# Performance work log

Hardware: AMD Instinct MI355X
Metric: run time of the kernel (lower is better)

Reference implementation:

```python
import jax, jax.numpy as jnp
import numpy as np

B, L, D = 2, 1024, 2048
E, K = 8, 2
H, HS = 1408, 2816


def setup_inputs() -> dict:
    key = jax.random.key(0)
    ks = jax.random.split(key, 9)
    s = 0.02  # param init scale
    return {
        "x": jax.random.normal(ks[0], (B, L, D), dtype=jnp.float32),
        "gate_w": jax.random.normal(ks[1], (E, D), dtype=jnp.float32) * s,
        "w_gate": jax.random.normal(ks[2], (E, D, H), dtype=jnp.float32) * s,
        "w_up": jax.random.normal(ks[3], (E, D, H), dtype=jnp.float32) * s,
        "w_down": jax.random.normal(ks[4], (E, H, D), dtype=jnp.float32) * s,
        "shgate_w": jax.random.normal(ks[5], (D,), dtype=jnp.float32) * s,
        "shw_gate": jax.random.normal(ks[6], (D, HS), dtype=jnp.float32) * s,
        "shw_up": jax.random.normal(ks[7], (D, HS), dtype=jnp.float32) * s,
        "shw_down": jax.random.normal(ks[8], (HS, D), dtype=jnp.float32) * s,
    }


def reference(x, gate_w, w_gate, w_up, w_down, shgate_w, shw_gate, shw_up, shw_down):
    b, l, d = x.shape
    xf = x.reshape(-1, d)  # [T, D]

    # --- router: softmax over expert logits, top-k, renormalize ---
    logits = jnp.einsum("td,ed->te", xf.astype(jnp.float32), gate_w)
    probs = jax.nn.softmax(logits.astype(jnp.float32), axis=-1)  # [T, E]
    weights, indices = jax.lax.top_k(probs, K)                   # [T, K]
    weights = (weights / weights.sum(-1, keepdims=True)).astype(x.dtype)

    # per-token combine weight for each expert: sum of top-k weights routed to e
    onehot = jax.nn.one_hot(indices, E, dtype=x.dtype)           # [T, K, E]
    combine = jnp.einsum("tk,tke->te", weights, onehot)          # [T, E]

    # --- experts (dense vectorized equivalent of masked gather/scatter loop) ---
    g = jnp.einsum("td,edh->teh", xf, w_gate)
    u = jnp.einsum("td,edh->teh", xf, w_up)
    h = jax.nn.silu(g) * u                                       # [T, E, H]
    # fused down-proj + weighted combine; accumulate in fp32 like the original
    out = jnp.einsum("teh,ehd,te->td", h.astype(jnp.float32),
                     w_down.astype(jnp.float32), combine.astype(jnp.float32))

    # --- shared expert with sigmoid gate ---
    sgate = jax.nn.sigmoid(xf @ shgate_w)[:, None]               # [T, 1]
    sh = (jax.nn.silu(xf @ shw_gate) * (xf @ shw_up)) @ shw_down  # [T, D]
    out = out + (sgate * sh).astype(jnp.float32)

    return out.astype(x.dtype).reshape(b, l, d)
```

## Files before the change

kernel.cpp:

```cpp
#include <hip/hip_runtime.h>
#include <hip/hip_bf16.h>
#include <math.h>

#define T_TOK 2048
#define Dd    2048
#define Ee    8
#define Hh    1408
#define HSs   2816
#define CAP   1024

typedef __attribute__((ext_vector_type(8))) __bf16 bf16x8;
typedef __attribute__((ext_vector_type(4))) __bf16 bf16x4;
typedef __attribute__((ext_vector_type(2))) __bf16 bf16x2;
typedef __attribute__((ext_vector_type(4))) float  f32x4;

#define MFMA(a, b, c) __builtin_amdgcn_mfma_f32_16x16x32_bf16(a, b, c, 0, 0, 0)

__device__ __forceinline__ void async_copy16(const __bf16* g, __bf16* l) {
    __builtin_amdgcn_global_load_lds(
        (const __attribute__((address_space(1))) unsigned int*)g,
        (__attribute__((address_space(3))) unsigned int*)l, 16, 0, 0);
}

__global__ void init_cnt(int* __restrict__ cnt) {
    if (threadIdx.x < Ee) cnt[threadIdx.x] = 0;
}

__global__ __launch_bounds__(256) void router_kernel(
    const float* __restrict__ x, const float* __restrict__ gate_w,
    const float* __restrict__ shgate_w,
    int* __restrict__ cnt, int* __restrict__ ptok, int* __restrict__ pslot,
    float* __restrict__ pw, float* __restrict__ sgate)
{
    const int t = blockIdx.x;
    const int tid = threadIdx.x;
    const float* xt = x + (size_t)t * Dd;

    float acc[Ee];
#pragma unroll
    for (int e = 0; e < Ee; e++) acc[e] = 0.f;
    float accs = 0.f;

    for (int d = tid; d < Dd; d += 256) {
        float xv = xt[d];
#pragma unroll
        for (int e = 0; e < Ee; e++) acc[e] += xv * gate_w[e * Dd + d];
        accs += xv * shgate_w[d];
    }

    __shared__ float red[Ee + 1][256];
#pragma unroll
    for (int e = 0; e < Ee; e++) red[e][tid] = acc[e];
    red[Ee][tid] = accs;
    __syncthreads();

    for (int s = 128; s > 0; s >>= 1) {
        if (tid < s) {
#pragma unroll
            for (int e = 0; e <= Ee; e++) red[e][tid] += red[e][tid + s];
        }
        __syncthreads();
    }

    if (tid == 0) {
        float l0 = -1e30f, l1 = -1e30f;
        int i0 = 0, i1 = 0;
#pragma unroll
        for (int e = 0; e < Ee; e++) {
            float v = red[e][0];
            if (v > l0) { l1 = l0; i1 = i0; l0 = v; i0 = e; }
            else if (v > l1) { l1 = v; i1 = e; }
        }
        float w0 = 1.f / (1.f + expf(l1 - l0));
        float w1 = 1.f - w0;

        int p0 = atomicAdd(&cnt[i0], 1);
        if (p0 < CAP) {
            ptok[i0 * CAP + p0] = t; pslot[i0 * CAP + p0] = 2 * t;
            pw[i0 * CAP + p0] = w0;
        }
        int p1 = atomicAdd(&cnt[i1], 1);
        if (p1 < CAP) {
            ptok[i1 * CAP + p1] = t; pslot[i1 * CAP + p1] = 2 * t + 1;
            pw[i1 * CAP + p1] = w1;
        }
        sgate[t] = 1.f / (1.f + expf(-red[Ee][0]));
    }
}

__global__ __launch_bounds__(256) void cvt_x(const float* __restrict__ src,
                                             __bf16* __restrict__ dst)
{
    int i = blockIdx.x * 256 + threadIdx.x;
    float4 v = ((const float4*)src)[i];
    bf16x4 o = { (__bf16)v.x, (__bf16)v.y, (__bf16)v.z, (__bf16)v.w };
    ((bf16x4*)dst)[i] = o;
}

__global__ __launch_bounds__(256) void transpose_cvt(
    const float* __restrict__ src, __bf16* __restrict__ dst, int R, int C)
{
    src += (size_t)blockIdx.z * R * C;
    dst += (size_t)blockIdx.z * R * C;
    __shared__ float tile[64][65];
    const int tid = threadIdx.x, tx = tid & 63, ty = tid >> 6;
    const int c0 = blockIdx.x * 64, r0 = blockIdx.y * 64;
#pragma unroll
    for (int j = 0; j < 16; j++) {
        int r = j * 4 + ty;
        tile[r][tx] = src[(size_t)(r0 + r) * C + c0 + tx];
    }
    __syncthreads();
    const int rp = (tid & 31) * 2;
    const int cg = tid >> 5;
#pragma unroll
    for (int j = 0; j < 8; j++) {
        int c = j * 8 + cg;
        bf16x2 v = { (__bf16)tile[rp][c], (__bf16)tile[rp + 1][c] };
        *(bf16x2*)&dst[(size_t)(c0 + c) * R + r0 + rp] = v;
    }
}

__global__ __launch_bounds__(256, 3) void gateup_all(
    const __bf16* __restrict__ xb,
    const __bf16* __restrict__ wgT, const __bf16* __restrict__ wuT,
    const __bf16* __restrict__ shwgT, const __bf16* __restrict__ shwuT,
    const int* __restrict__ cnt, const int* __restrict__ ptok,
    __bf16* __restrict__ hq, __bf16* __restrict__ shh)
{
    const int bx = blockIdx.x;
    const int tid = threadIdx.x, lane = tid & 63, wave = tid >> 6;
    const int wr = wave >> 1, wc = wave & 1;
    const int lm = lane & 15, lq = lane >> 4;

    bool sh;
    int m0, h0, n, e = 0;
    const __bf16 *bg_mat, *bu_mat;
    if (bx < 1408) {
        sh = false;
        int mtg = bx / 22, ht = bx - mtg * 22;
        e = mtg >> 3; m0 = (mtg & 7) * 128; h0 = ht * 64;
        n = cnt[e]; if (n > CAP) n = CAP;
        if (m0 >= n) return;
        bg_mat = wgT + (size_t)e * Hh * Dd;
        bu_mat = wuT + (size_t)e * Hh * Dd;
    } else {
        sh = true;
        int s = bx - 1408;
        int mt = s / 44, ht = s - mt * 44;
        m0 = mt * 128; h0 = ht * 64; n = T_TOK;
        bg_mat = shwgT; bu_mat = shwuT;
    }

    __shared__ __align__(16) __bf16 stage[8192];
    __shared__ int tok_s[128];

    if (tid < 128) {
        int i = m0 + tid;
        if (sh) tok_s[tid] = i;
        else { int ic = i < n ? i : n - 1; tok_s[tid] = ptok[e * CAP + ic]; }
    }
    __syncthreads();

    const __bf16* pa0 = xb + (size_t)tok_s[wave * 16 + lm] * Dd + lq * 8;
    const __bf16* pa1 = xb + (size_t)tok_s[64 + wave * 16 + lm] * Dd + lq * 8;
    const __bf16* pbg = bg_mat + (size_t)(h0 + wave * 16 + lm) * Dd + lq * 8;
    const __bf16* pbu = bu_mat + (size_t)(h0 + wave * 16 + lm) * Dd + lq * 8;
    __bf16* la0 = stage + wave * 512 + lane * 8;
    __bf16* la1 = stage + (4 + wave) * 512 + lane * 8;
    __bf16* lbg = stage + 4096 + wave * 512 + lane * 8;
    __bf16* lbu = stage + 6144 + wave * 512 + lane * 8;

    f32x4 acc[4][4] = {};

    for (int k0 = 0; k0 < Dd; k0 += 32) {
        async_copy16(pa0, la0); async_copy16(pa1, la1);
        async_copy16(pbg, lbg); async_copy16(pbu, lbu);
        pa0 += 32; pa1 += 32; pbg += 32; pbu += 32;
        __syncthreads();
        bf16x8 af[4], bfr[4];
        const __bf16* bbase = stage + (wc ? 6144 : 4096);
#pragma unroll
        for (int i = 0; i < 4; i++)
            af[i] = *(const bf16x8*)(stage + (wr * 4 + i) * 512 + lane * 8);
#pragma unroll
        for (int j = 0; j < 4; j++)
            bfr[j] = *(const bf16x8*)(bbase + j * 512 + lane * 8);
#pragma unroll
        for (int i = 0; i < 4; i++)
#pragma unroll
            for (int j = 0; j < 4; j++)
                acc[i][j] = MFMA(af[i], bfr[j], acc[i][j]);
        __syncthreads();
    }

    if (wc == 1) {
#pragma unroll
        for (int i = 0; i < 4; i++)
#pragma unroll
            for (int j = 0; j < 4; j++) {
                bf16x4 uv;
#pragma unroll
                for (int r = 0; r < 4; r++) uv[r] = (__bf16)acc[i][j][r];
                *(bf16x4*)(stage + ((wr * 4 + i) * 4 + j) * 256 + lane * 4) = uv;
            }
    }
    __syncthreads();
    if (wc == 0) {
#pragma unroll
        for (int i = 0; i < 4; i++)
#pragma unroll
            for (int j = 0; j < 4; j++) {
                bf16x4 uv = *(const bf16x4*)(stage + ((wr * 4 + i) * 4 + j) * 256 + lane * 4);
                int col = h0 + j * 16 + lm;
#pragma unroll
                for (int r = 0; r < 4; r++) {
                    int grow = m0 + wr * 64 + i * 16 + lq * 4 + r;
                    if (!sh && grow >= n) continue;
                    float g = acc[i][j][r], u = (float)uv[r];
                    float hv = g / (1.f + __expf(-g)) * u;
                    if (sh) shh[(size_t)grow * HSs + col] = (__bf16)hv;
                    else    hq[((size_t)e * CAP + grow) * Hh + col] = (__bf16)hv;
                }
            }
    }
}

__global__ __launch_bounds__(256, 3) void down_all(
    const __bf16* __restrict__ hq, const __bf16* __restrict__ wdT,
    const __bf16* __restrict__ shh, const __bf16* __restrict__ shwdT,
    const int* __restrict__ cnt, const int* __restrict__ pslot,
    const float* __restrict__ pw, const float* __restrict__ sgate,
    float* __restrict__ eo, float* __restrict__ out)
{
    const int bx = blockIdx.x;
    const int tid = threadIdx.x, lane = tid & 63, wave = tid >> 6;
    const int wr = wave >> 1, wc = wave & 1;
    const int lm = lane & 15, lq = lane >> 4;

    bool sh;
    int m0, n0, n, e = 0, kdim;
    if (bx < 1024) {
        sh = false;
        e = bx >> 7; m0 = ((bx >> 4) & 7) * 128; n0 = (bx & 15) * 128;
        n = cnt[e]; if (n > CAP) n = CAP;
        if (m0 >= n) return;
        kdim = Hh;
    } else {
        sh = true;
        int s = bx - 1024;
        m0 = (s >> 4) * 128; n0 = (s & 15) * 128; n = T_TOK;
        kdim = HSs;
    }

    __shared__ __align__(16) __bf16 stage[8192];
    __shared__ int   slot_s[128];
    __shared__ float w_s[128];

    if (!sh && tid < 128) {
        int i = m0 + tid; int ic = i < n ? i : n - 1;
        slot_s[tid] = pslot[e * CAP + ic];
        w_s[tid] = (i < n) ? pw[e * CAP + ic] : 0.f;
    }

    int ar0 = m0 + wave * 16 + lm, ar1 = m0 + 64 + wave * 16 + lm;
    const __bf16 *pa0, *pa1, *pb0, *pb1;
    if (sh) {
        pa0 = shh + (size_t)ar0 * HSs + lq * 8;
        pa1 = shh + (size_t)ar1 * HSs + lq * 8;
        pb0 = shwdT + (size_t)(n0 + wave * 16 + lm) * HSs + lq * 8;
        pb1 = shwdT + (size_t)(n0 + 64 + wave * 16 + lm) * HSs + lq * 8;
    } else {
        int a0c = ar0 < n ? ar0 : n - 1;
        int a1c = ar1 < n ? ar1 : n - 1;
        pa0 = hq + ((size_t)e * CAP + a0c) * Hh + lq * 8;
        pa1 = hq + ((size_t)e * CAP + a1c) * Hh + lq * 8;
        pb0 = wdT + ((size_t)e * Dd + n0 + wave * 16 + lm) * Hh + lq * 8;
        pb1 = wdT + ((size_t)e * Dd + n0 + 64 + wave * 16 + lm) * Hh + lq * 8;
    }
    __bf16* la0 = stage + wave * 512 + lane * 8;
    __bf16* la1 = stage + (4 + wave) * 512 + lane * 8;
    __bf16* lb0 = stage + 4096 + wave * 512 + lane * 8;
    __bf16* lb1 = stage + 4096 + (4 + wave) * 512 + lane * 8;

    f32x4 acc[4][4] = {};

    for (int k0 = 0; k0 < kdim; k0 += 32) {
        async_copy16(pa0, la0); async_copy16(pa1, la1);
        async_copy16(pb0, lb0); async_copy16(pb1, lb1);
        pa0 += 32; pa1 += 32; pb0 += 32; pb1 += 32;
        __syncthreads();
        bf16x8 af[4], bfr[4];
#pragma unroll
        for (int i = 0; i < 4; i++)
            af[i] = *(const bf16x8*)(stage + (wr * 4 + i) * 512 + lane * 8);
#pragma unroll
        for (int j = 0; j < 4; j++)
            bfr[j] = *(const bf16x8*)(stage + 4096 + (wc * 4 + j) * 512 + lane * 8);
#pragma unroll
        for (int i = 0; i < 4; i++)
#pragma unroll
            for (int j = 0; j < 4; j++)
                acc[i][j] = MFMA(af[i], bfr[j], acc[i][j]);
        __syncthreads();
    }

#pragma unroll
    for (int i = 0; i < 4; i++)
#pragma unroll
        for (int r = 0; r < 4; r++) {
            int rloc = wr * 64 + i * 16 + lq * 4 + r;
            if (sh) {
                int t = m0 + rloc;
                float sg = sgate[t];
#pragma unroll
                for (int j = 0; j < 4; j++)
                    out[(size_t)t * Dd + n0 + (wc * 4 + j) * 16 + lm] = sg * acc[i][j][r];
            } else if (m0 + rloc < n) {
                int   slot = slot_s[rloc];
                float w    = w_s[rloc];
#pragma unroll
                for (int j = 0; j < 4; j++)
                    eo[(size_t)slot * Dd + n0 + (wc * 4 + j) * 16 + lm] = w * acc[i][j][r];
            }
        }
}

__global__ __launch_bounds__(256) void combine_kernel(
    const float* __restrict__ eo, float* __restrict__ out)
{
    int i4 = blockIdx.x * 256 + threadIdx.x;
    int t = i4 >> 9;
    int c = i4 & 511;
    float4 o = ((const float4*)out)[i4];
    float4 a = ((const float4*)(eo + (size_t)(2 * t) * Dd))[c];
    float4 b = ((const float4*)(eo + (size_t)(2 * t + 1) * Dd))[c];
    o.x += a.x + b.x; o.y += a.y + b.y; o.z += a.z + b.z; o.w += a.w + b.w;
    ((float4*)out)[i4] = o;
}

extern "C" void kernel_launch(void* const* d_in, const int* in_sizes, int n_in,
                              void* d_out, int out_size, void* d_ws, size_t ws_size,
                              hipStream_t stream) {
    const float* x        = (const float*)d_in[0];
    const float* gate_w   = (const float*)d_in[1];
    const float* w_gate   = (const float*)d_in[2];
    const float* w_up     = (const float*)d_in[3];
    const float* w_down   = (const float*)d_in[4];
    const float* shgate_w = (const float*)d_in[5];
    const float* shw_gate = (const float*)d_in[6];
    const float* shw_up   = (const float*)d_in[7];
    const float* shw_down = (const float*)d_in[8];
    float* out = (float*)d_out;

    char* ws = (char*)d_ws;
    size_t off = 0;
    auto alloc = [&](size_t bytes) { char* p = ws + off; off = (off + bytes + 255) & ~(size_t)255; return p; };
    int*    cnt    = (int*)   alloc(Ee * 4);
    int*    ptok   = (int*)   alloc(Ee * CAP * 4);
    int*    pslot  = (int*)   alloc(Ee * CAP * 4);
    float*  pw     = (float*) alloc(Ee * CAP * 4);
    float*  sgate  = (float*) alloc(T_TOK * 4);
    __bf16* xb     = (__bf16*)alloc((size_t)T_TOK * Dd * 2);
    __bf16* wgT    = (__bf16*)alloc((size_t)Ee * Hh * Dd * 2);
    __bf16* wuT    = (__bf16*)alloc((size_t)Ee * Hh * Dd * 2);
    __bf16* wdT    = (__bf16*)alloc((size_t)Ee * Dd * Hh * 2);
    __bf16* shwgT  = (__bf16*)alloc((size_t)HSs * Dd * 2);
    __bf16* shwuT  = (__bf16*)alloc((size_t)HSs * Dd * 2);
    __bf16* shwdT  = (__bf16*)alloc((size_t)Dd * HSs * 2);
    __bf16* hq     = (__bf16*)alloc((size_t)Ee * CAP * Hh * 2);
    __bf16* shh    = (__bf16*)alloc((size_t)T_TOK * HSs * 2);
    float*  eo     = (float*) alloc((size_t)T_TOK * 2 * Dd * 4);

    dim3 b256(256);

    init_cnt<<<dim3(1), dim3(64), 0, stream>>>(cnt);
    router_kernel<<<dim3(T_TOK), b256, 0, stream>>>(
        x, gate_w, shgate_w, cnt, ptok, pslot, pw, sgate);
    cvt_x<<<dim3(T_TOK * Dd / 4 / 256), b256, 0, stream>>>(x, xb);
    transpose_cvt<<<dim3(Hh / 64, Dd / 64, Ee), b256, 0, stream>>>(w_gate, wgT, Dd, Hh);
    transpose_cvt<<<dim3(Hh / 64, Dd / 64, Ee), b256, 0, stream>>>(w_up, wuT, Dd, Hh);
    transpose_cvt<<<dim3(Dd / 64, Hh / 64, Ee), b256, 0, stream>>>(w_down, wdT, Hh, Dd);
    transpose_cvt<<<dim3(HSs / 64, Dd / 64, 1), b256, 0, stream>>>(shw_gate, shwgT, Dd, HSs);
    transpose_cvt<<<dim3(HSs / 64, Dd / 64, 1), b256, 0, stream>>>(shw_up, shwuT, Dd, HSs);
    transpose_cvt<<<dim3(Dd / 64, HSs / 64, 1), b256, 0, stream>>>(shw_down, shwdT, HSs, Dd);

    gateup_all<<<dim3(1408 + 704), b256, 0, stream>>>(
        xb, wgT, wuT, shwgT, shwuT, cnt, ptok, hq, shh);
    down_all<<<dim3(1024 + 256), b256, 0, stream>>>(
        hq, wdT, shh, shwdT, cnt, pslot, pw, sgate, eo, out);
    combine_kernel<<<dim3(T_TOK * Dd / 4 / 256), b256, 0, stream>>>(eo, out);
}
```

Baseline: 811.7 us.

## Restructure MoE pipeline: merged prep kernel, 128x128 gate/up GEMM, separate SiLU pass

Six transpose-convert launches are merged into one prep kernel. The gate/up GEMM now computes a plain 128x128 tile over a concatenated gate|up output, with a K step of 64, and writes raw bf16 results to a temporary buffer. A separate silu_mul kernel then builds the hidden activations. The down GEMM also moves to a K step of 64, and both GEMMs reorder blocks so M tiles vary fastest, which should reuse weight tiles in cache. Together these are meant to cut per-iteration barrier overhead and launch count. The cost is an extra round-trip of the gate/up intermediate through global memory, doubled LDS use, and a workspace region shared between the gate/up buffer and eo.

```diff
diff --git a/kernel.cpp b/kernel.cpp
--- a/kernel.cpp
+++ b/kernel.cpp
@@ -97,14 +97,31 @@
     ((bf16x4*)dst)[i] = o;
 }
 
-__global__ __launch_bounds__(256) void transpose_cvt(
-    const float* __restrict__ src, __bf16* __restrict__ dst, int R, int C)
-{
-    src += (size_t)blockIdx.z * R * C;
-    dst += (size_t)blockIdx.z * R * C;
+__global__ __launch_bounds__(256) void prep_all(
+    const float* __restrict__ w_gate, const float* __restrict__ w_up,
+    const float* __restrict__ w_down, const float* __restrict__ shw_gate,
+    const float* __restrict__ shw_up, const float* __restrict__ shw_down,
+    __bf16* __restrict__ wgT, __bf16* __restrict__ wuT, __bf16* __restrict__ wdT,
+    __bf16* __restrict__ shwgT, __bf16* __restrict__ shwuT, __bf16* __restrict__ shwdT)
+{
+    int t = blockIdx.x;
+    const float* src; __bf16* dst; int R, C;
+    if (t < 5632)        { int b = t / 704; t -= b * 704; R = Dd; C = Hh;
+                           src = w_gate + (size_t)b * R * C; dst = wgT + (size_t)b * R * C; }
+    else if (t < 11264)  { t -= 5632; int b = t / 704; t -= b * 704; R = Dd; C = Hh;
+                           src = w_up + (size_t)b * R * C; dst = wuT + (size_t)b * R * C; }
+    else if (t < 16896)  { t -= 11264; int b = t / 704; t -= b * 704; R = Hh; C = Dd;
+                           src = w_down + (size_t)b * R * C; dst = wdT + (size_t)b * R * C; }
+    else if (t < 18304)  { t -= 16896; R = Dd; C = HSs; src = shw_gate; dst = shwgT; }
+    else if (t < 19712)  { t -= 18304; R = Dd; C = HSs; src = shw_up;   dst = shwuT; }
+    else                 { t -= 19712; R = HSs; C = Dd; src = shw_down; dst = shwdT; }
+
+    const int tC = C >> 6;
+    const int rt = t / tC, ct = t - rt * tC;
+    const int r0 = rt * 64, c0 = ct * 64;
+
     __shared__ float tile[64][65];
     const int tid = threadIdx.x, tx = tid & 63, ty = tid >> 6;
-    const int c0 = blockIdx.x * 64, r0 = blockIdx.y * 64;
 #pragma unroll
     for (int j = 0; j < 16; j++) {
         int r = j * 4 + ty;
@@ -121,12 +138,12 @@
     }
 }
 
-__global__ __launch_bounds__(256, 3) void gateup_all(
+__global__ __launch_bounds__(256, 3) void gateup_gemm(
     const __bf16* __restrict__ xb,
     const __bf16* __restrict__ wgT, const __bf16* __restrict__ wuT,
     const __bf16* __restrict__ shwgT, const __bf16* __restrict__ shwuT,
     const int* __restrict__ cnt, const int* __restrict__ ptok,
-    __bf16* __restrict__ hq, __bf16* __restrict__ shh)
+    __bf16* __restrict__ gu_e, __bf16* __restrict__ gu_s)
 {
     const int bx = blockIdx.x;
     const int tid = threadIdx.x, lane = tid & 63, wave = tid >> 6;
@@ -134,25 +151,25 @@
     const int lm = lane & 15, lq = lane >> 4;
 
     bool sh;
-    int m0, h0, n, e = 0;
-    const __bf16 *bg_mat, *bu_mat;
+    int m0, nt, n, e = 0;
+    const __bf16* Bbase;
     if (bx < 1408) {
         sh = false;
-        int mtg = bx / 22, ht = bx - mtg * 22;
-        e = mtg >> 3; m0 = (mtg & 7) * 128; h0 = ht * 64;
+        e = bx / 176; int rem = bx - e * 176;
+        nt = rem >> 3; m0 = (rem & 7) * 128;
         n = cnt[e]; if (n > CAP) n = CAP;
         if (m0 >= n) return;
-        bg_mat = wgT + (size_t)e * Hh * Dd;
-        bu_mat = wuT + (size_t)e * Hh * Dd;
+        Bbase = (nt < 11) ? wgT + (size_t)e * Hh * Dd + (size_t)(nt * 128) * Dd
+                          : wuT + (size_t)e * Hh * Dd + (size_t)(nt * 128 - 1408) * Dd;
     } else {
         sh = true;
         int s = bx - 1408;
-        int mt = s / 44, ht = s - mt * 44;
-        m0 = mt * 128; h0 = ht * 64; n = T_TOK;
-        bg_mat = shwgT; bu_mat = shwuT;
-    }
-
-    __shared__ __align__(16) __bf16 stage[8192];
+        nt = s >> 4; m0 = (s & 15) * 128; n = T_TOK;
+        Bbase = (nt < 22) ? shwgT + (size_t)(nt * 128) * Dd
+                          : shwuT + (size_t)(nt * 128 - 2816) * Dd;
+    }
+
+    __shared__ __align__(16) __bf16 stage[16384];
     __shared__ int tok_s[128];
 
     if (tid < 128) {
@@ -164,69 +181,85 @@
 
     const __bf16* pa0 = xb + (size_t)tok_s[wave * 16 + lm] * Dd + lq * 8;
     const __bf16* pa1 = xb + (size_t)tok_s[64 + wave * 16 + lm] * Dd + lq * 8;
-    const __bf16* pbg = bg_mat + (size_t)(h0 + wave * 16 + lm) * Dd + lq * 8;
-    const __bf16* pbu = bu_mat + (size_t)(h0 + wave * 16 + lm) * Dd + lq * 8;
-    __bf16* la0 = stage + wave * 512 + lane * 8;
-    __bf16* la1 = stage + (4 + wave) * 512 + lane * 8;
-    __bf16* lbg = stage + 4096 + wave * 512 + lane * 8;
-    __bf16* lbu = stage + 6144 + wave * 512 + lane * 8;
+    const __bf16* pb0 = Bbase + (size_t)(wave * 16 + lm) * Dd + lq * 8;
+    const __bf16* pb1 = Bbase + (size_t)(64 + wave * 16 + lm) * Dd + lq * 8;
+    __bf16* la0 = stage + wave * 1024 + lane * 8;
+    __bf16* la1 = stage + (4 + wave) * 1024 + lane * 8;
+    __bf16* lb0 = stage + 8192 + wave * 1024 + lane * 8;
+    __bf16* lb1 = stage + 8192 + (4 + wave) * 1024 + lane * 8;
 
     f32x4 acc[4][4] = {};
 
-    for (int k0 = 0; k0 < Dd; k0 += 32) {
-        async_copy16(pa0, la0); async_copy16(pa1, la1);
-        async_copy16(pbg, lbg); async_copy16(pbu, lbu);
-        pa0 += 32; pa1 += 32; pbg += 32; pbu += 32;
+    for (int k0 = 0; k0 < Dd; k0 += 64) {
+        async_copy16(pa0 + k0, la0);       async_copy16(pa0 + k0 + 32, la0 + 512);
+        async_copy16(pa1 + k0, la1);       async_copy16(pa1 + k0 + 32, la1 + 512);
+        async_copy16(pb0 + k0, lb0);       async_copy16(pb0 + k0 + 32, lb0 + 512);
+        async_copy16(pb1 + k0, lb1);       async_copy16(pb1 + k0 + 32, lb1 + 512);
         __syncthreads();
-        bf16x8 af[4], bfr[4];
-        const __bf16* bbase = stage + (wc ? 6144 : 4096);
-#pragma unroll
-        for (int i = 0; i < 4; i++)
-            af[i] = *(const bf16x8*)(stage + (wr * 4 + i) * 512 + lane * 8);
-#pragma unroll
-        for (int j = 0; j < 4; j++)
-            bfr[j] = *(const bf16x8*)(bbase + j * 512 + lane * 8);
-#pragma unroll
-        for (int i = 0; i < 4; i++)
+#pragma unroll
+        for (int kk = 0; kk < 2; kk++) {
+            bf16x8 af[4], bfr[4];
+#pragma unroll
+            for (int i = 0; i < 4; i++)
+                af[i] = *(const bf16x8*)(stage + (wr * 4 + i) * 1024 + kk * 512 + lane * 8);
 #pragma unroll
             for (int j = 0; j < 4; j++)
-                acc[i][j] = MFMA(af[i], bfr[j], acc[i][j]);
+                bfr[j] = *(const bf16x8*)(stage + 8192 + (wc * 4 + j) * 1024 + kk * 512 + lane * 8);
+#pragma unroll
+            for (int i = 0; i < 4; i++)
+#pragma unroll
+                for (int j = 0; j < 4; j++)
+                    acc[i][j] = MFMA(af[i], bfr[j], acc[i][j]);
+        }
         __syncthreads();
     }
 
-    if (wc == 1) {
-#pragma unroll
-        for (int i = 0; i < 4; i++)
+    const int colbase = nt * 128 + wc * 64;
+#pragma unroll
+    for (int i = 0; i < 4; i++)
+#pragma unroll
+        for (int r = 0; r < 4; r++) {
+            int row = m0 + wr * 64 + i * 16 + lq * 4 + r;
+            if (!sh && row >= n) continue;
 #pragma unroll
             for (int j = 0; j < 4; j++) {
-                bf16x4 uv;
-#pragma unroll
-                for (int r = 0; r < 4; r++) uv[r] = (__bf16)acc[i][j][r];
-                *(bf16x4*)(stage + ((wr * 4 + i) * 4 + j) * 256 + lane * 4) = uv;
+                int col = colbase + j * 16 + lm;
+                if (sh) gu_s[(size_t)row * 5632 + col] = (__bf16)acc[i][j][r];
+                else    gu_e[((size_t)e * CAP + row) * 2816 + col] = (__bf16)acc[i][j][r];
             }
-    }
-    __syncthreads();
-    if (wc == 0) {
-#pragma unroll
-        for (int i = 0; i < 4; i++)
-#pragma unroll
-            for (int j = 0; j < 4; j++) {
-                bf16x4 uv = *(const bf16x4*)(stage + ((wr * 4 + i) * 4 + j) * 256 + lane * 4);
-                int col = h0 + j * 16 + lm;
-#pragma unroll
-                for (int r = 0; r < 4; r++) {
-                    int grow = m0 + wr * 64 + i * 16 + lq * 4 + r;
-                    if (!sh && grow >= n) continue;
-                    float g = acc[i][j][r], u = (float)uv[r];
-                    float hv = g / (1.f + __expf(-g)) * u;
-                    if (sh) shh[(size_t)grow * HSs + col] = (__bf16)hv;
-                    else    hq[((size_t)e * CAP + grow) * Hh + col] = (__bf16)hv;
-                }
-            }
-    }
-}
-
-__global__ __launch_bounds__(256, 3) void down_all(
+        }
+}
+
+__global__ __launch_bounds__(256) void silu_mul(
+    const __bf16* __restrict__ gu_e, const __bf16* __restrict__ gu_s,
+    __bf16* __restrict__ hq, __bf16* __restrict__ shh)
+{
+    const int bx = blockIdx.x, tid = threadIdx.x;
+    bf16x8 g8, u8;
+    __bf16* dst;
+    if (bx < 5632) {
+        int i = bx * 256 + tid;
+        int row = i / 176, c = i - row * 176;
+        g8 = *(const bf16x8*)(gu_e + (size_t)row * 2816 + c * 8);
+        u8 = *(const bf16x8*)(gu_e + (size_t)row * 2816 + 1408 + c * 8);
+        dst = hq + (size_t)row * 1408 + c * 8;
+    } else {
+        int i = (bx - 5632) * 256 + tid;
+        int row = i / 352, c = i - row * 352;
+        g8 = *(const bf16x8*)(gu_s + (size_t)row * 5632 + c * 8);
+        u8 = *(const bf16x8*)(gu_s + (size_t)row * 5632 + 2816 + c * 8);
+        dst = shh + (size_t)row * 2816 + c * 8;
+    }
+    bf16x8 o;
+#pragma unroll
+    for (int k = 0; k < 8; k++) {
+        float g = (float)g8[k], u = (float)u8[k];
+        o[k] = (__bf16)(g / (1.f + __expf(-g)) * u);
+    }
+    *(bf16x8*)dst = o;
+}
+
+__global__ __launch_bounds__(256, 3) void down_gemm(
     const __bf16* __restrict__ hq, const __bf16* __restrict__ wdT,
     const __bf16* __restrict__ shh, const __bf16* __restrict__ shwdT,
     const int* __restrict__ cnt, const int* __restrict__ pslot,
@@ -242,18 +275,19 @@
     int m0, n0, n, e = 0, kdim;
     if (bx < 1024) {
         sh = false;
-        e = bx >> 7; m0 = ((bx >> 4) & 7) * 128; n0 = (bx & 15) * 128;
+        e = bx >> 7; int rem = bx & 127;
+        n0 = (rem >> 3) * 128; m0 = (rem & 7) * 128;
         n = cnt[e]; if (n > CAP) n = CAP;
         if (m0 >= n) return;
         kdim = Hh;
     } else {
         sh = true;
         int s = bx - 1024;
-        m0 = (s >> 4) * 128; n0 = (s & 15) * 128; n = T_TOK;
+        n0 = (s >> 4) * 128; m0 = (s & 15) * 128; n = T_TOK;
         kdim = HSs;
     }
 
-    __shared__ __align__(16) __bf16 stage[8192];
+    __shared__ __align__(16) __bf16 stage[16384];
     __shared__ int   slot_s[128];
     __shared__ float w_s[128];
 
@@ -278,30 +312,34 @@
         pb0 = wdT + ((size_t)e * Dd + n0 + wave * 16 + lm) * Hh + lq * 8;
         pb1 = wdT + ((size_t)e * Dd + n0 + 64 + wave * 16 + lm) * Hh + lq * 8;
     }
-    __bf16* la0 = stage + wave * 512 + lane * 8;
-    __bf16* la1 = stage + (4 + wave) * 512 + lane * 8;
-    __bf16* lb0 = stage + 4096 + wave * 512 + lane * 8;
-    __bf16* lb1 = stage + 4096 + (4 + wave) * 512 + lane * 8;
+    __bf16* la0 = stage + wave * 1024 + lane * 8;
+    __bf16* la1 = stage + (4 + wave) * 1024 + lane * 8;
+    __bf16* lb0 = stage + 8192 + wave * 1024 + lane * 8;
+    __bf16* lb1 = stage + 8192 + (4 + wave) * 1024 + lane * 8;
 
     f32x4 acc[4][4] = {};
 
-    for (int k0 = 0; k0 < kdim; k0 += 32) {
-        async_copy16(pa0, la0); async_copy16(pa1, la1);
-        async_copy16(pb0, lb0); async_copy16(pb1, lb1);
-        pa0 += 32; pa1 += 32; pb0 += 32; pb1 += 32;
+    for (int k0 = 0; k0 < kdim; k0 += 64) {
+        async_copy16(pa0 + k0, la0);       async_copy16(pa0 + k0 + 32, la0 + 512);
+        async_copy16(pa1 + k0, la1);       async_copy16(pa1 + k0 + 32, la1 + 512);
+        async_copy16(pb0 + k0, lb0);       async_copy16(pb0 + k0 + 32, lb0 + 512);
+        async_copy16(pb1 + k0, lb1);       async_copy16(pb1 + k0 + 32, lb1 + 512);
         __syncthreads();
-        bf16x8 af[4], bfr[4];
-#pragma unroll
-        for (int i = 0; i < 4; i++)
-            af[i] = *(const bf16x8*)(stage + (wr * 4 + i) * 512 + lane * 8);
-#pragma unroll
-        for (int j = 0; j < 4; j++)
-            bfr[j] = *(const bf16x8*)(stage + 4096 + (wc * 4 + j) * 512 + lane * 8);
-#pragma unroll
-        for (int i = 0; i < 4; i++)
+#pragma unroll
+        for (int kk = 0; kk < 2; kk++) {
+            bf16x8 af[4], bfr[4];
+#pragma unroll
+            for (int i = 0; i < 4; i++)
+                af[i] = *(const bf16x8*)(stage + (wr * 4 + i) * 1024 + kk * 512 + lane * 8);
 #pragma unroll
             for (int j = 0; j < 4; j++)
-                acc[i][j] = MFMA(af[i], bfr[j], acc[i][j]);
+                bfr[j] = *(const bf16x8*)(stage + 8192 + (wc * 4 + j) * 1024 + kk * 512 + lane * 8);
+#pragma unroll
+            for (int i = 0; i < 4; i++)
+#pragma unroll
+                for (int j = 0; j < 4; j++)
+                    acc[i][j] = MFMA(af[i], bfr[j], acc[i][j]);
+        }
         __syncthreads();
     }
 
@@ -315,13 +353,13 @@
                 float sg = sgate[t];
 #pragma unroll
                 for (int j = 0; j < 4; j++)
-                    out[(size_t)t * Dd + n0 + (wc * 4 + j) * 16 + lm] = sg * acc[i][j][r];
+                    out[(size_t)t * Dd + n0 + wc * 64 + j * 16 + lm] = sg * acc[i][j][r];
             } else if (m0 + rloc < n) {
                 int   slot = slot_s[rloc];
                 float w    = w_s[rloc];
 #pragma unroll
                 for (int j = 0; j < 4; j++)
-                    eo[(size_t)slot * Dd + n0 + (wc * 4 + j) * 16 + lm] = w * acc[i][j][r];
+                    eo[(size_t)slot * Dd + n0 + wc * 64 + j * 16 + lm] = w * acc[i][j][r];
             }
         }
 }
@@ -370,7 +408,10 @@
     __bf16* shwdT  = (__bf16*)alloc((size_t)Dd * HSs * 2);
     __bf16* hq     = (__bf16*)alloc((size_t)Ee * CAP * Hh * 2);
     __bf16* shh    = (__bf16*)alloc((size_t)T_TOK * HSs * 2);
-    float*  eo     = (float*) alloc((size_t)T_TOK * 2 * Dd * 4);
+    char*   region = alloc((size_t)Ee * CAP * 2816 * 2 + (size_t)T_TOK * 5632 * 2);
+    __bf16* gu_e   = (__bf16*)region;
+    __bf16* gu_s   = (__bf16*)(region + (size_t)Ee * CAP * 2816 * 2);
+    float*  eo     = (float*)region;
 
     dim3 b256(256);
 
@@ -378,16 +419,14 @@
     router_kernel<<<dim3(T_TOK), b256, 0, stream>>>(
         x, gate_w, shgate_w, cnt, ptok, pslot, pw, sgate);
     cvt_x<<<dim3(T_TOK * Dd / 4 / 256), b256, 0, stream>>>(x, xb);
-    transpose_cvt<<<dim3(Hh / 64, Dd / 64, Ee), b256, 0, stream>>>(w_gate, wgT, Dd, Hh);
-    transpose_cvt<<<dim3(Hh / 64, Dd / 64, Ee), b256, 0, stream>>>(w_up, wuT, Dd, Hh);
-    transpose_cvt<<<dim3(Dd / 64, Hh / 64, Ee), b256, 0, stream>>>(w_down, wdT, Hh, Dd);
-    transpose_cvt<<<dim3(HSs / 64, Dd / 64, 1), b256, 0, stream>>>(shw_gate, shwgT, Dd, HSs);
-    transpose_cvt<<<dim3(HSs / 64, Dd / 64, 1), b256, 0, stream>>>(shw_up, shwuT, Dd, HSs);
-    transpose_cvt<<<dim3(Dd / 64, HSs / 64, 1), b256, 0, stream>>>(shw_down, shwdT, HSs, Dd);
-
-    gateup_all<<<dim3(1408 + 704), b256, 0, stream>>>(
-        xb, wgT, wuT, shwgT, shwuT, cnt, ptok, hq, shh);
-    down_all<<<dim3(1024 + 256), b256, 0, stream>>>(
+    prep_all<<<dim3(21120), b256, 0, stream>>>(
+        w_gate, w_up, w_down, shw_gate, shw_up, shw_down,
+        wgT, wuT, wdT, shwgT, shwuT, shwdT);
+
+    gateup_gemm<<<dim3(1408 + 704), b256, 0, stream>>>(
+        xb, wgT, wuT, shwgT, shwuT, cnt, ptok, gu_e, gu_s);
+    silu_mul<<<dim3(5632 + 2816), b256, 0, stream>>>(gu_e, gu_s, hq, shh);
+    down_gemm<<<dim3(1024 + 256), b256, 0, stream>>>(
         hq, wdT, shh, shwdT, cnt, pslot, pw, sgate, eo, out);
     combine_kernel<<<dim3(T_TOK * Dd / 4 / 256), b256, 0, stream>>>(eo, out);
 }
```

Result: slower. 864.9 us (+6.6%).
